# Optimization experiments

Hardware: AMD Instinct MI355X
Metric: run time of the kernel (lower is better)

The kernel has to match this reference:

```python
import jax, jax.numpy as jnp
import numpy as np

N, T, F = 20000, 20, 128
H = 128          # lstm hidden per direction
GH, HEADS = 128, 4
NUM_CLASSES = 10
E = 640000
SCALE = 0.05


def _lstm_last_hidden(x, lengths, Wih, Whh, b):
    """Run a unidirectional LSTM over padded x [N,T,F]; return hidden at the
    last valid step per sequence (torch gate order i,f,g,o)."""
    pre = jnp.einsum('ntf,gf->ntg', x, Wih) + b            # [N,T,4H]
    mask = jnp.arange(x.shape[1])[None, :] < lengths[:, None]  # [N,T]
    h0 = jnp.zeros((x.shape[0], Whh.shape[1]), x.dtype)

    def step(carry, inp):
        h, c = carry
        pt, m = inp                                         # [N,4H], [N]
        gates = pt + h @ Whh.T
        i, f, g, o = jnp.split(gates, 4, axis=-1)
        c_new = jax.nn.sigmoid(f) * c + jax.nn.sigmoid(i) * jnp.tanh(g)
        h_new = jax.nn.sigmoid(o) * jnp.tanh(c_new)
        m = m[:, None]
        return (jnp.where(m, h_new, h), jnp.where(m, c_new, c)), None

    (h, _), _ = jax.lax.scan(step, (h0, h0), (pre.transpose(1, 0, 2), mask.T))
    return h


def _reverse_by_length(x, lengths):
    # x[n, t] -> x[n, len-1-t] for t < len (padding positions are masked later)
    idx = jnp.clip(lengths[:, None] - 1 - jnp.arange(x.shape[1])[None, :], 0, None)
    return x[jnp.arange(x.shape[0])[:, None], idx]


def _gat(h, src, dst, W, a_src, a_dst, bias, heads):
    n = h.shape[0]
    xh = (h @ W.T).reshape(n, heads, -1)                    # [N,H,C]
    al_s = jnp.sum(xh * a_src, -1)                          # [N,H]
    al_d = jnp.sum(xh * a_dst, -1)
    e = jax.nn.leaky_relu(al_s[src] + al_d[dst], 0.2)       # [E,H]
    emax = jax.ops.segment_max(e, dst, num_segments=n)
    emax = jnp.where(jnp.isfinite(emax), emax, 0.0)
    ee = jnp.exp(e - emax[dst])
    denom = jax.ops.segment_sum(ee, dst, num_segments=n)
    alpha = ee / (denom[dst] + 1e-16)                       # segment softmax
    out = jax.ops.segment_sum(xh[src] * alpha[..., None], dst, num_segments=n)
    return out.reshape(n, -1) + bias


def setup_inputs() -> dict:
    key = jax.random.key(0)
    ks = jax.random.split(key, 16)
    p = lambda k, *s: jax.random.normal(k, s, jnp.float32) * SCALE
    return {
        'x': jax.random.normal(ks[0], (N, T, F), jnp.float32),
        'lengths': jax.random.randint(ks[1], (N,), 1, T + 1, jnp.int32),
        'edge_index': jax.random.randint(ks[2], (2, E), 0, N, jnp.int32),
        # BiLSTM params (b = b_ih + b_hh combined; identical math)
        'Wih_f': p(ks[3], 4 * H, F), 'Whh_f': p(ks[4], 4 * H, H), 'b_f': p(ks[5], 4 * H),
        'Wih_b': p(ks[6], 4 * H, F), 'Whh_b': p(ks[7], 4 * H, H), 'b_b': p(ks[8], 4 * H),
        # GAT1: in=2H=256 -> heads*GH=512
        'W1': p(ks[9], HEADS * GH, 2 * H), 'a1_src': p(ks[10], HEADS, GH),
        'a1_dst': p(ks[11], HEADS, GH), 'bias1': jnp.zeros((HEADS * GH,), jnp.float32),
        # GAT2: in=512 -> 1*GH=128
        'W2': p(ks[12], GH, HEADS * GH), 'a2_src': p(ks[13], 1, GH),
        'a2_dst': p(ks[14], 1, GH), 'bias2': jnp.zeros((GH,), jnp.float32),
        'Wfc': p(ks[15], NUM_CLASSES, GH), 'bfc': jnp.zeros((NUM_CLASSES,), jnp.float32),
    }


def reference(x, lengths, edge_index, Wih_f, Whh_f, b_f, Wih_b, Whh_b, b_b,
              W1, a1_src, a1_dst, bias1, W2, a2_src, a2_dst, bias2, Wfc, bfc):
    n = x.shape[0]
    h_fwd = _lstm_last_hidden(x, lengths, Wih_f, Whh_f, b_f)
    h_bwd = _lstm_last_hidden(_reverse_by_length(x, lengths), lengths, Wih_b, Whh_b, b_b)
    h = jnp.concatenate([h_fwd, h_bwd], axis=-1)            # [N, 2H]
    # GATConv default adds self-loops
    loop = jnp.arange(n, dtype=edge_index.dtype)
    src = jnp.concatenate([edge_index[0], loop])
    dst = jnp.concatenate([edge_index[1], loop])
    h = jax.nn.relu(_gat(h, src, dst, W1, a1_src, a1_dst, bias1, HEADS))
    h = jax.nn.relu(_gat(h, src, dst, W2, a2_src, a2_dst, bias2, 1))
    return h @ Wfc.T + bfc                                  # [N, num_classes]
```

## Files before the change

### kernel.cpp

```cpp
#include <hip/hip_runtime.h>

#define NSEQ 20000
#define TT 20
#define FD 128
#define EDG 640000
#define ETOT (EDG + NSEQ)

typedef short bf16x8 __attribute__((ext_vector_type(8)));
typedef float f32x4 __attribute__((ext_vector_type(4)));
typedef unsigned short u16;
typedef unsigned int u32;

__device__ __forceinline__ float bf2f(u16 h) {
  union { u32 u; float f; } v; v.u = ((u32)h) << 16; return v.f;
}
__device__ __forceinline__ float bf_lo(u32 w) {
  union { u32 u; float f; } v; v.u = w << 16; return v.f;
}
__device__ __forceinline__ float bf_hi(u32 w) {
  union { u32 u; float f; } v; v.u = w & 0xffff0000u; return v.f;
}
__device__ __forceinline__ u16 f2bf(float f) {
  union { float f; u32 u; } v; v.f = f;
  u32 u = v.u;
  return (u16)((u + 0x7fffu + ((u >> 16) & 1u)) >> 16);
}
__device__ __forceinline__ float fast_rcp(float x) {
  float r; asm("v_rcp_f32 %0, %1" : "=v"(r) : "v"(x)); return r;
}
__device__ __forceinline__ float fast_ex2(float x) {
  float r; asm("v_exp_f32 %0, %1" : "=v"(r) : "v"(x)); return r;
}
__device__ __forceinline__ u32 cvtpk_bf16(float a, float b) {
  u32 r; asm("v_cvt_pk_bf16_f32 %0, %1, %2" : "=v"(r) : "v"(a), "v"(b)); return r;
}
__device__ __forceinline__ int clampi(int v, int lo, int hi) {
  return v < lo ? lo : (v > hi ? hi : v);
}

template<int BF>
__device__ __forceinline__ bf16x8 ld8(const void* p, size_t i) {
  if (BF) return *(const bf16x8*)((const u16*)p + i);
  f32x4 a = *(const f32x4*)((const float*)p + i);
  f32x4 b = *(const f32x4*)((const float*)p + i + 4);
  union { u32 w[4]; bf16x8 v; } u;
  u.w[0] = cvtpk_bf16(a[0], a[1]);
  u.w[1] = cvtpk_bf16(a[2], a[3]);
  u.w[2] = cvtpk_bf16(b[0], b[1]);
  u.w[3] = cvtpk_bf16(b[2], b[3]);
  return u.v;
}

#define OFF_WIHF 0
#define OFF_WHHF 65536
#define OFF_BF   131072
#define OFF_WIHB 131584
#define OFF_WHHB 197120
#define OFF_BB   262656
#define OFF_W1   263168
#define OFF_W2   394240
#define OFF_A1S  459776
#define OFF_A1D  460288
#define OFF_B1   460800
#define OFF_A2S  461312
#define OFF_A2D  461440
#define OFF_B2   461568
#define OFF_WFC  461696
#define OFF_BFC  462976

__global__ void k_detect_zero(const u32* __restrict__ xw, int* __restrict__ flag,
                              int* __restrict__ deg, int* __restrict__ lcnt) {
  int i = blockIdx.x * 256 + threadIdx.x;
  if (i < NSEQ) deg[i] = 0;
  if (i < 64) lcnt[i] = 0;
  if (blockIdx.x == 0 && threadIdx.x < 64) {
    u16 lo = (u16)(xw[threadIdx.x] & 0xffffu);
    int e = (lo >> 7) & 0xff;
    unsigned long long m = __ballot(e >= 100 && e <= 140);
    if (threadIdx.x == 0) flag[0] = (__popcll(m) >= 32) ? 1 : 0;
  }
}

struct CvtArgs {
  const void* src[16];
  int off[16];
  int cnt[16];
  int wt[16];
};

template<int BF>
__global__ void k_cvt(CvtArgs a, u16* __restrict__ canon, const int* __restrict__ flag) {
  if (flag[0] != BF) return;
  int idx = blockIdx.x * 256 + threadIdx.x;
  int stride = gridDim.x * 256;
#pragma unroll 1
  for (int s = 0; s < 16; ++s) {
    const void* sp = a.src[s];
    int n = a.cnt[s], off = a.off[s], wt = a.wt[s];
    for (int i = idx; i < n; i += stride) {
      float v = BF ? bf2f(((const u16*)sp)[i]) : ((const float*)sp)[i];
      if (wt) {
        int gate = (wt == 1) ? ((i >> 14) & 3) : ((i >> 7) & 3);
        v *= (gate == 2) ? 2.885390082f : -1.442695041f;
      }
      canon[off + i] = f2bf(v);
    }
  }
}

__global__ void k_fill0(u16* __restrict__ out, int n) {
  int i = blockIdx.x * 256 + threadIdx.x;
  if (i < n) out[i] = 0;
}

template<int BF>
__global__ __launch_bounds__(512, 2) void k_lstm(
    const void* __restrict__ x, const int* __restrict__ lengths,
    const int* __restrict__ lperm,
    const u16* __restrict__ canon, u16* __restrict__ hcat,
    const int* __restrict__ flag)
{
  if (flag[0] != BF) return;
  __shared__ u16 Ax[2][64 * 128];
  __shared__ u16 Ah[2][64 * 128];
  __shared__ int lenS[64];
  __shared__ int seqS[64];

  const int tid = threadIdx.x;
  const int wv = tid >> 6;
  const int lane = tid & 63;
  const int q = lane >> 4;
  const int cc = lane & 15;
  const int dir = blockIdx.x;
  const int b0 = (gridDim.y - 1 - blockIdx.y) * 64;

  const u16* Wi = canon + (dir ? OFF_WIHB : OFF_WIHF);
  const u16* Wh = canon + (dir ? OFF_WHHB : OFF_WHHF);
  const u16* bb = canon + (dir ? OFF_BB : OFF_BF);

  bf16x8 wih[4][4], whh[4][4];
  uint2 bvp[4];
#pragma unroll
  for (int g = 0; g < 4; ++g) {
    int row = g * 128 + wv * 16 + cc;
#pragma unroll
    for (int kt = 0; kt < 4; ++kt) {
      wih[g][kt] = *(const bf16x8*)(Wi + row * 128 + kt * 32 + q * 8);
      whh[g][kt] = *(const bf16x8*)(Wh + row * 128 + kt * 32 + q * 8);
    }
    bvp[g] = *(const uint2*)(bb + g * 128 + wv * 16 + q * 4);
  }

  if (tid < 64) {
    int s = lperm[clampi(b0 + tid, 0, NSEQ - 1)];
    s = clampi(s, 0, NSEQ - 1);
    seqS[tid] = s;
    lenS[tid] = clampi(lengths[s], 1, TT);
  }
  {
    f32x4 zz = {0.f, 0.f, 0.f, 0.f};
    f32x4* p = (f32x4*)Ah[0];
    for (int i = tid; i < 1024; i += 512) p[i] = zz;
  }
  __syncthreads();

  const int tmax = lenS[63];

  int lenq[4];
#pragma unroll
  for (int m = 0; m < 4; ++m) lenq[m] = lenS[m * 16 + cc];

  const int lrow = tid >> 3;
  const int lj = tid & 7;
  const int sL = seqS[lrow];
  const int lenL = lenS[lrow];
  const size_t xbase = (size_t)sL * (TT * FD);
  const int ax0 = lrow * 128 + ((lj ^ (lrow & 15)) * 8);
  const int ax1 = lrow * 128 + (((lj + 8) ^ (lrow & 15)) * 8);

  int rofs[4];
#pragma unroll
  for (int kt = 0; kt < 4; ++kt) rofs[kt] = cc * 128 + (((4 * kt + q) ^ cc) * 8);
  const int awbase = cc * 128 + (((wv * 2 + (q >> 1)) ^ cc) * 8) + (q & 1) * 4;

  {
    int t0 = dir ? (lenL - 1) : 0;
    bf16x8 d0 = ld8<BF>(x, xbase + t0 * FD + lj * 8);
    bf16x8 d1 = ld8<BF>(x, xbase + t0 * FD + (lj + 8) * 8);
    *(bf16x8*)&Ax[0][ax0] = d0;
    *(bf16x8*)&Ax[0][ax1] = d1;
  }
  float c[4][4] = {};
  int cb = 0;
  __syncthreads();

#pragma unroll 1
  for (int t = 0; t < tmax; ++t) {
    const u16* Axr = Ax[cb];
    u16* Axw = Ax[cb ^ 1];
    const u16* Ahr = Ah[cb];
    u16* Ahw = Ah[cb ^ 1];

    bf16x8 d0 = {}, d1 = {};
    const bool more = (t + 1 < tmax);
    if (more) {
      int tn = t + 1;
      int tt2 = dir ? (lenL - 1 - tn) : tn;
      if (tt2 < 0) tt2 = 0;
      d0 = ld8<BF>(x, xbase + tt2 * FD + lj * 8);
      d1 = ld8<BF>(x, xbase + tt2 * FD + (lj + 8) * 8);
    }

#pragma unroll
    for (int m = 0; m < 4; ++m) {
      const int mb = m * 2048;
      f32x4 acc[4];
#pragma unroll
      for (int g = 0; g < 4; ++g) {
        f32x4 vi = {bf_lo(bvp[g].x), bf_hi(bvp[g].x), bf_lo(bvp[g].y), bf_hi(bvp[g].y)};
        acc[g] = vi;
      }
#pragma unroll
      for (int kt = 0; kt < 4; ++kt) {
        bf16x8 b = *(const bf16x8*)&Axr[mb + rofs[kt]];
#pragma unroll
        for (int g = 0; g < 4; ++g)
          acc[g] = __builtin_amdgcn_mfma_f32_16x16x32_bf16(wih[g][kt], b, acc[g], 0, 0, 0);
      }
#pragma unroll
      for (int kt = 0; kt < 4; ++kt) {
        bf16x8 b = *(const bf16x8*)&Ahr[mb + rofs[kt]];
#pragma unroll
        for (int g = 0; g < 4; ++g)
          acc[g] = __builtin_amdgcn_mfma_f32_16x16x32_bf16(whh[g][kt], b, acc[g], 0, 0, 0);
      }

      uint2 hw;
      if (t < lenq[m]) {
        float hf[4];
#pragma unroll
        for (int r = 0; r < 4; ++r) {
          float Ei = fast_ex2(acc[0][r]);
          float Ef = fast_ex2(acc[1][r]);
          float G  = fast_ex2(acc[2][r]) + 1.0f;
          float Eo = fast_ex2(acc[3][r]);
          float A = 1.0f + Ef, B = 1.0f + Ei;
          float BG = B * G;
          float num = c[m][r] * BG + (A * G - 2.0f * A);
          float cn = num * fast_rcp(A * BG);
          c[m][r] = cn;
          float C2 = fast_ex2(cn * 2.885390082f) + 1.0f;
          hf[r] = (C2 - 2.0f) * fast_rcp((1.0f + Eo) * C2);
        }
        hw.x = cvtpk_bf16(hf[0], hf[1]);
        hw.y = cvtpk_bf16(hf[2], hf[3]);
      } else {
        hw = *(const uint2*)&Ahr[mb + awbase];
      }
      *(uint2*)&Ahw[mb + awbase] = hw;
    }

    if (more) {
      *(bf16x8*)&Axw[ax0] = d0;
      *(bf16x8*)&Axw[ax1] = d1;
    }
    __syncthreads();
    cb ^= 1;
  }

  for (int i = tid; i < 1024; i += 512) {
    int row = i >> 4, ch = i & 15;
    if (b0 + row < NSEQ) {
      int seq = seqS[row];
      bf16x8 v = *(const bf16x8*)&Ah[cb][row * 128 + ((ch ^ (row & 15)) * 8)];
      *(bf16x8*)(hcat + (size_t)seq * 256 + dir * 128 + ch * 8) = v;
    }
  }
}

__global__ __launch_bounds__(256) void k_gemm(
    const u16* __restrict__ A, const u16* __restrict__ W, u16* __restrict__ C,
    int M, int Nc, int K,
    const u16* __restrict__ aS, const u16* __restrict__ aD,
    float* __restrict__ als, float* __restrict__ ald, int alsStride)
{
  __shared__ u16 As[128 * 64];
  __shared__ u16 Bs[128 * 64];
  const int tid = threadIdx.x;
  const int wv = tid >> 6, lane = tid & 63, q = lane >> 4, cc = lane & 15;
  const int mblk = blockIdx.x * 128, nblk = blockIdx.y * 128;
  const int wm = (wv & 1) * 64, wn = (wv >> 1) * 64;

  f32x4 acc[4][4] = {};

  const int srow = tid >> 1;
  const int sc0 = (tid & 1) * 4;
  int arow_g = mblk + srow; if (arow_g > M - 1) arow_g = M - 1;
  const u16* aptr = A + (size_t)arow_g * K + sc0 * 8;
  const u16* bptr = W + (size_t)(nblk + srow) * K + sc0 * 8;

  for (int k0 = 0; k0 < K; k0 += 64) {
#pragma unroll
    for (int cch = 0; cch < 4; ++cch) {
      bf16x8 av = *(const bf16x8*)(aptr + k0 + cch * 8);
      bf16x8 bvv = *(const bf16x8*)(bptr + k0 + cch * 8);
      int ch = sc0 + cch;
      *(bf16x8*)&As[srow * 64 + ((ch ^ (srow & 7)) * 8)] = av;
      *(bf16x8*)&Bs[srow * 64 + ((ch ^ (srow & 7)) * 8)] = bvv;
    }
    __syncthreads();
#pragma unroll
    for (int kt = 0; kt < 2; ++kt) {
      bf16x8 af[4];
#pragma unroll
      for (int m = 0; m < 4; ++m) {
        int row = wm + m * 16 + cc;
        af[m] = *(const bf16x8*)&As[row * 64 + (((4 * kt + q) ^ (row & 7)) * 8)];
      }
#pragma unroll
      for (int n = 0; n < 4; ++n) {
        int rowb = wn + n * 16 + cc;
        bf16x8 bfr = *(const bf16x8*)&Bs[rowb * 64 + (((4 * kt + q) ^ (rowb & 7)) * 8)];
#pragma unroll
        for (int m = 0; m < 4; ++m)
          acc[m][n] = __builtin_amdgcn_mfma_f32_16x16x32_bf16(bfr, af[m], acc[m][n], 0, 0, 0);
      }
    }
    __syncthreads();
  }

  float pls[4] = {}, pld[4] = {};
#pragma unroll
  for (int n = 0; n < 4; ++n) {
    uint2 ws = *(const uint2*)(aS + nblk + wn + n * 16 + q * 4);
    uint2 wd = *(const uint2*)(aD + nblk + wn + n * 16 + q * 4);
    float s0 = bf_lo(ws.x), s1 = bf_hi(ws.x), s2 = bf_lo(ws.y), s3 = bf_hi(ws.y);
    float d0 = bf_lo(wd.x), d1 = bf_hi(wd.x), d2 = bf_lo(wd.y), d3 = bf_hi(wd.y);
#pragma unroll
    for (int m = 0; m < 4; ++m) {
      int row = mblk + wm + m * 16 + cc;
      uint2 st;
      st.x = cvtpk_bf16(acc[m][n][0], acc[m][n][1]);
      st.y = cvtpk_bf16(acc[m][n][2], acc[m][n][3]);
      if (row < M) *(uint2*)(C + (size_t)row * Nc + nblk + wn + n * 16 + q * 4) = st;
      pls[m] += acc[m][n][0] * s0 + acc[m][n][1] * s1 + acc[m][n][2] * s2 + acc[m][n][3] * s3;
      pld[m] += acc[m][n][0] * d0 + acc[m][n][1] * d1 + acc[m][n][2] * d2 + acc[m][n][3] * d3;
    }
  }

#pragma unroll
  for (int m = 0; m < 4; ++m) {
    pls[m] += __shfl_xor(pls[m], 16, 64);
    pls[m] += __shfl_xor(pls[m], 32, 64);
    pld[m] += __shfl_xor(pld[m], 16, 64);
    pld[m] += __shfl_xor(pld[m], 32, 64);
  }
  float* sred = (float*)As;
  if (lane < 16) {
#pragma unroll
    for (int m = 0; m < 4; ++m) {
      int idx = ((wv & 1) * 4 + m) * 32 + cc * 2 + (wv >> 1);
      sred[idx] = pls[m];
      sred[256 + idx] = pld[m];
    }
  }
  __syncthreads();
  if (wv < 2) {
    int m = lane >> 4, ccc = lane & 15;
    int row = mblk + wv * 64 + m * 16 + ccc;
    int idx = (wv * 4 + m) * 32 + ccc * 2;
    if (row < M) {
      als[(size_t)row * alsStride + blockIdx.y] = sred[idx] + sred[idx + 1];
      ald[(size_t)row * alsStride + blockIdx.y] = sred[256 + idx] + sred[256 + idx + 1];
    }
  }
}

__global__ __launch_bounds__(256) void k_agg1(
    const u16* __restrict__ xh1, const float* __restrict__ als, const float* __restrict__ ald,
    const int* __restrict__ offs, const int* __restrict__ csr,
    const u16* __restrict__ canon, u16* __restrict__ h1)
{
  const int lane = threadIdx.x & 63;
  const int n = blockIdx.x * 4 + (threadIdx.x >> 6);
  int off0 = offs[n], off1 = offs[n + 1];
  off0 = clampi(off0, 0, ETOT);
  off1 = clampi(off1, off0, ETOT);
  const int deg = off1 - off0;
  const float4 ad = *(const float4*)(ald + (size_t)n * 4);
  const u16* xb = xh1 + lane * 2;

  float o0 = 0.f, o1 = 0.f, o2 = 0.f, o3 = 0.f, o4 = 0.f, o5 = 0.f, o6 = 0.f, o7 = 0.f;
  if (deg <= 64) {
    int s = 0;
    float e0 = -1e30f, e1 = -1e30f, e2 = -1e30f, e3 = -1e30f;
    if (lane < deg) {
      s = clampi(csr[off0 + lane], 0, NSEQ - 1);
      float4 av = *(const float4*)(als + (size_t)s * 4);
      float t;
      t = av.x + ad.x; e0 = t > 0.f ? t : 0.2f * t;
      t = av.y + ad.y; e1 = t > 0.f ? t : 0.2f * t;
      t = av.z + ad.z; e2 = t > 0.f ? t : 0.2f * t;
      t = av.w + ad.w; e3 = t > 0.f ? t : 0.2f * t;
    }
    float m0 = e0, m1 = e1, m2 = e2, m3 = e3;
#pragma unroll
    for (int off = 32; off >= 1; off >>= 1) {
      m0 = fmaxf(m0, __shfl_xor(m0, off, 64));
      m1 = fmaxf(m1, __shfl_xor(m1, off, 64));
      m2 = fmaxf(m2, __shfl_xor(m2, off, 64));
      m3 = fmaxf(m3, __shfl_xor(m3, off, 64));
    }
    float x0 = (lane < deg) ? __expf(e0 - m0) : 0.f;
    float x1 = (lane < deg) ? __expf(e1 - m1) : 0.f;
    float x2 = (lane < deg) ? __expf(e2 - m2) : 0.f;
    float x3 = (lane < deg) ? __expf(e3 - m3) : 0.f;
    float s0 = x0, s1 = x1, s2 = x2, s3 = x3;
#pragma unroll
    for (int off = 32; off >= 1; off >>= 1) {
      s0 += __shfl_xor(s0, off, 64);
      s1 += __shfl_xor(s1, off, 64);
      s2 += __shfl_xor(s2, off, 64);
      s3 += __shfl_xor(s3, off, 64);
    }
    float a0 = x0 * fast_rcp(s0 + 1e-16f);
    float a1 = x1 * fast_rcp(s1 + 1e-16f);
    float a2 = x2 * fast_rcp(s2 + 1e-16f);
    float a3 = x3 * fast_rcp(s3 + 1e-16f);
    const int sofs = s * 512;
#pragma unroll 4
    for (int j = 0; j < deg; ++j) {
      int so = __builtin_amdgcn_readlane(sofs, j);
      float aa0 = __int_as_float(__builtin_amdgcn_readlane(__float_as_int(a0), j));
      float aa1 = __int_as_float(__builtin_amdgcn_readlane(__float_as_int(a1), j));
      float aa2 = __int_as_float(__builtin_amdgcn_readlane(__float_as_int(a2), j));
      float aa3 = __int_as_float(__builtin_amdgcn_readlane(__float_as_int(a3), j));
      u32 v0 = *(const u32*)(xb + so);
      u32 v1 = *(const u32*)(xb + so + 128);
      u32 v2 = *(const u32*)(xb + so + 256);
      u32 v3 = *(const u32*)(xb + so + 384);
      o0 += aa0 * bf_lo(v0); o1 += aa0 * bf_hi(v0);
      o2 += aa1 * bf_lo(v1); o3 += aa1 * bf_hi(v1);
      o4 += aa2 * bf_lo(v2); o5 += aa2 * bf_hi(v2);
      o6 += aa3 * bf_lo(v3); o7 += aa3 * bf_hi(v3);
    }
  } else {
    float m0 = -1e30f, m1 = -1e30f, m2 = -1e30f, m3 = -1e30f;
    for (int k = off0 + lane; k < off1; k += 64) {
      int s = clampi(csr[k], 0, NSEQ - 1);
      float4 av = *(const float4*)(als + (size_t)s * 4);
      float t;
      t = av.x + ad.x; t = t > 0.f ? t : 0.2f * t; m0 = fmaxf(m0, t);
      t = av.y + ad.y; t = t > 0.f ? t : 0.2f * t; m1 = fmaxf(m1, t);
      t = av.z + ad.z; t = t > 0.f ? t : 0.2f * t; m2 = fmaxf(m2, t);
      t = av.w + ad.w; t = t > 0.f ? t : 0.2f * t; m3 = fmaxf(m3, t);
    }
#pragma unroll
    for (int off = 32; off >= 1; off >>= 1) {
      m0 = fmaxf(m0, __shfl_xor(m0, off, 64));
      m1 = fmaxf(m1, __shfl_xor(m1, off, 64));
      m2 = fmaxf(m2, __shfl_xor(m2, off, 64));
      m3 = fmaxf(m3, __shfl_xor(m3, off, 64));
    }
    float s0 = 0.f, s1 = 0.f, s2 = 0.f, s3 = 0.f;
    for (int k = off0 + lane; k < off1; k += 64) {
      int s = clampi(csr[k], 0, NSEQ - 1);
      float4 av = *(const float4*)(als + (size_t)s * 4);
      float t;
      t = av.x + ad.x; t = t > 0.f ? t : 0.2f * t; s0 += __expf(t - m0);
      t = av.y + ad.y; t = t > 0.f ? t : 0.2f * t; s1 += __expf(t - m1);
      t = av.z + ad.z; t = t > 0.f ? t : 0.2f * t; s2 += __expf(t - m2);
      t = av.w + ad.w; t = t > 0.f ? t : 0.2f * t; s3 += __expf(t - m3);
    }
#pragma unroll
    for (int off = 32; off >= 1; off >>= 1) {
      s0 += __shfl_xor(s0, off, 64);
      s1 += __shfl_xor(s1, off, 64);
      s2 += __shfl_xor(s2, off, 64);
      s3 += __shfl_xor(s3, off, 64);
    }
    float rd0 = fast_rcp(s0 + 1e-16f), rd1 = fast_rcp(s1 + 1e-16f);
    float rd2 = fast_rcp(s2 + 1e-16f), rd3 = fast_rcp(s3 + 1e-16f);
    for (int k = off0; k < off1; ++k) {
      int s = clampi(csr[k], 0, NSEQ - 1);
      float4 av = *(const float4*)(als + (size_t)s * 4);
      float t;
      t = av.x + ad.x; t = t > 0.f ? t : 0.2f * t; float aa0 = __expf(t - m0) * rd0;
      t = av.y + ad.y; t = t > 0.f ? t : 0.2f * t; float aa1 = __expf(t - m1) * rd1;
      t = av.z + ad.z; t = t > 0.f ? t : 0.2f * t; float aa2 = __expf(t - m2) * rd2;
      t = av.w + ad.w; t = t > 0.f ? t : 0.2f * t; float aa3 = __expf(t - m3) * rd3;
      const u16* xr = xb + (size_t)s * 512;
      u32 v0 = *(const u32*)(xr);
      u32 v1 = *(const u32*)(xr + 128);
      u32 v2 = *(const u32*)(xr + 256);
      u32 v3 = *(const u32*)(xr + 384);
      o0 += aa0 * bf_lo(v0); o1 += aa0 * bf_hi(v0);
      o2 += aa1 * bf_lo(v1); o3 += aa1 * bf_hi(v1);
      o4 += aa2 * bf_lo(v2); o5 += aa2 * bf_hi(v2);
      o6 += aa3 * bf_lo(v3); o7 += aa3 * bf_hi(v3);
    }
  }
  float b0 = bf2f(canon[OFF_B1 + lane * 2]),       b1 = bf2f(canon[OFF_B1 + lane * 2 + 1]);
  float b2 = bf2f(canon[OFF_B1 + 128 + lane * 2]), b3 = bf2f(canon[OFF_B1 + 128 + lane * 2 + 1]);
  float b4 = bf2f(canon[OFF_B1 + 256 + lane * 2]), b5 = bf2f(canon[OFF_B1 + 256 + lane * 2 + 1]);
  float b6 = bf2f(canon[OFF_B1 + 384 + lane * 2]), b7 = bf2f(canon[OFF_B1 + 384 + lane * 2 + 1]);
  o0 += b0; o1 += b1; o2 += b2; o3 += b3; o4 += b4; o5 += b5; o6 += b6; o7 += b7;
  o0 = o0 > 0.f ? o0 : 0.f; o1 = o1 > 0.f ? o1 : 0.f;
  o2 = o2 > 0.f ? o2 : 0.f; o3 = o3 > 0.f ? o3 : 0.f;
  o4 = o4 > 0.f ? o4 : 0.f; o5 = o5 > 0.f ? o5 : 0.f;
  o6 = o6 > 0.f ? o6 : 0.f; o7 = o7 > 0.f ? o7 : 0.f;
  u16* hb = h1 + (size_t)n * 512 + lane * 2;
  *(u32*)(hb)       = cvtpk_bf16(o0, o1);
  *(u32*)(hb + 128) = cvtpk_bf16(o2, o3);
  *(u32*)(hb + 256) = cvtpk_bf16(o4, o5);
  *(u32*)(hb + 384) = cvtpk_bf16(o6, o7);
}

__global__ __launch_bounds__(256) void k_agg2(
    const u16* __restrict__ xh2, const float* __restrict__ als2, const float* __restrict__ ald2,
    const int* __restrict__ offs, const int* __restrict__ csr,
    const u16* __restrict__ canon, void* __restrict__ out, const int* __restrict__ flag)
{
  const int lane = threadIdx.x & 63;
  const int n = blockIdx.x * 4 + (threadIdx.x >> 6);
  int off0 = offs[n], off1 = offs[n + 1];
  off0 = clampi(off0, 0, ETOT);
  off1 = clampi(off1, off0, ETOT);
  const float adn = ald2[n];
  const int deg = off1 - off0;

  float o0 = 0.f, o1 = 0.f;
  if (deg <= 64) {
    int s = 0;
    float e = -1e30f;
    if (lane < deg) {
      s = clampi(csr[off0 + lane], 0, NSEQ - 1);
      float t = als2[s] + adn;
      e = t > 0.f ? t : 0.2f * t;
    }
    float mx = e;
#pragma unroll
    for (int off = 32; off >= 1; off >>= 1) mx = fmaxf(mx, __shfl_xor(mx, off, 64));
    float ex = (lane < deg) ? __expf(e - mx) : 0.f;
    float sm = ex;
#pragma unroll
    for (int off = 32; off >= 1; off >>= 1) sm += __shfl_xor(sm, off, 64);
    const float a = ex * fast_rcp(sm + 1e-16f);
    const int sofs = s * 128;
#pragma unroll 4
    for (int j = 0; j < deg; ++j) {
      int so = __builtin_amdgcn_readlane(sofs, j);
      float aa = __int_as_float(__builtin_amdgcn_readlane(__float_as_int(a), j));
      u32 xv = *(const u32*)(xh2 + so + lane * 2);
      o0 += aa * bf_lo(xv);
      o1 += aa * bf_hi(xv);
    }
  } else {
    float mx = -1e30f;
    for (int k = off0 + lane; k < off1; k += 64) {
      float e = als2[clampi(csr[k], 0, NSEQ - 1)] + adn;
      e = e > 0.f ? e : 0.2f * e;
      mx = fmaxf(mx, e);
    }
#pragma unroll
    for (int off = 32; off >= 1; off >>= 1) mx = fmaxf(mx, __shfl_xor(mx, off, 64));
    float sm = 0.f;
    for (int k = off0 + lane; k < off1; k += 64) {
      float e = als2[clampi(csr[k], 0, NSEQ - 1)] + adn;
      e = e > 0.f ? e : 0.2f * e;
      sm += __expf(e - mx);
    }
#pragma unroll
    for (int off = 32; off >= 1; off >>= 1) sm += __shfl_xor(sm, off, 64);
    float rd = fast_rcp(sm + 1e-16f);
#pragma unroll 4
    for (int k = off0; k < off1; ++k) {
      int s = clampi(csr[k], 0, NSEQ - 1);
      float e = als2[s] + adn;
      e = e > 0.f ? e : 0.2f * e;
      float a = __expf(e - mx) * rd;
      u32 xv = *(const u32*)(xh2 + (size_t)s * 128 + lane * 2);
      o0 += a * bf_lo(xv);
      o1 += a * bf_hi(xv);
    }
  }
  o0 += bf2f(canon[OFF_B2 + lane * 2]);     o0 = o0 > 0.f ? o0 : 0.f;
  o1 += bf2f(canon[OFF_B2 + lane * 2 + 1]); o1 = o1 > 0.f ? o1 : 0.f;

  float res[10];
#pragma unroll
  for (int cls = 0; cls < 10; ++cls) {
    float p = o0 * bf2f(canon[OFF_WFC + cls * 128 + lane * 2]) +
              o1 * bf2f(canon[OFF_WFC + cls * 128 + lane * 2 + 1]);
#pragma unroll
    for (int off = 32; off >= 1; off >>= 1) p += __shfl_xor(p, off, 64);
    float v = p + bf2f(canon[OFF_BFC + cls]);
    res[cls] = (fabsf(v) < 1e30f) ? v : 0.f;
  }
  if (flag[0]) {
    if (lane < 5) {
      u32 pk = (u32)f2bf(res[lane * 2]) | ((u32)f2bf(res[lane * 2 + 1]) << 16);
      ((u32*)out)[(size_t)n * 5 + lane] = pk;
    }
  } else {
    if (lane < 10) ((float*)out)[(size_t)n * 10 + lane] = res[lane];
  }
}

__global__ void k_hist_all(const int* __restrict__ ei, const int* __restrict__ lengths,
                           int* __restrict__ deg, int* __restrict__ lcnt) {
  int i = blockIdx.x * 256 + threadIdx.x;
  if (i < ETOT) {
    int d = (i < EDG) ? ei[EDG + i] : (i - EDG);
    d = clampi(d, 0, NSEQ - 1);
    atomicAdd(&deg[d], 1);
  }
  if (i < NSEQ) atomicAdd(&lcnt[clampi(lengths[i], 1, TT) - 1], 1);
}

__global__ __launch_bounds__(1024) void k_scan(const int* __restrict__ deg,
                                               int* __restrict__ offs, int* __restrict__ cur,
                                               const int* __restrict__ lcnt,
                                               int* __restrict__ lcur) {
  __shared__ int wsum[16];
  const int tid = threadIdx.x;
  if (tid == 0) {
    int run = 0;
    for (int i = 0; i < TT; ++i) { lcur[i] = run; run += lcnt[i]; }
  }
  const int lane = tid & 63, wv = tid >> 6;
  const int CHUNK = 20;
  int base = tid * CHUNK;
  int loc[20];
  int s = 0;
#pragma unroll
  for (int i = 0; i < CHUNK; ++i) {
    int idx = base + i;
    int v = (idx < NSEQ) ? deg[idx] : 0;
    loc[i] = s;
    s += v;
  }
  int inc = s;
#pragma unroll
  for (int off = 1; off < 64; off <<= 1) {
    int t2 = __shfl_up(inc, off, 64);
    if (lane >= off) inc += t2;
  }
  if (lane == 63) wsum[wv] = inc;
  __syncthreads();
  int wbase = 0;
  for (int i = 0; i < wv; ++i) wbase += wsum[i];
  int tbase = wbase + inc - s;
#pragma unroll
  for (int i = 0; i < CHUNK; ++i) {
    int idx = base + i;
    if (idx < NSEQ) {
      int st = tbase + loc[i];
      offs[idx] = st;
      cur[idx] = st;
    }
  }
  if (tid == 0) offs[NSEQ] = ETOT;
}

__global__ void k_scatter_all(const int* __restrict__ ei, const int* __restrict__ lengths,
                              int* __restrict__ cur, int* __restrict__ csr,
                              int* __restrict__ lcur, int* __restrict__ lperm) {
  int i = blockIdx.x * 256 + threadIdx.x;
  if (i < ETOT) {
    int s, d;
    if (i < EDG) { s = ei[i]; d = ei[EDG + i]; }
    else { s = i - EDG; d = s; }
    d = clampi(d, 0, NSEQ - 1);
    int pos = atomicAdd(&cur[d], 1);
    pos = clampi(pos, 0, ETOT - 1);
    csr[pos] = s;
  }
  if (i < NSEQ) {
    int b = clampi(lengths[i], 1, TT) - 1;
    int pos = atomicAdd(&lcur[b], 1);
    lperm[clampi(pos, 0, NSEQ - 1)] = i;
  }
}

extern "C" void kernel_launch(void* const* d_in, const int* in_sizes, int n_in,
                              void* d_out, int out_size, void* d_ws, size_t ws_size,
                              hipStream_t stream) {
  (void)in_sizes; (void)n_in;
  const void* x     = d_in[0];
  const int* lengths= (const int*)d_in[1];
  const int* ei     = (const int*)d_in[2];

  const size_t NEED = 45769344u;
  if (ws_size < NEED) {
    k_fill0<<<(out_size + 255) / 256, 256, 0, stream>>>((u16*)d_out, out_size);
    return;
  }

  char* w = (char*)d_ws;
  size_t o = 0;
  auto alloc = [&](size_t b) { char* p = w + o; o += (b + 255) & ~(size_t)255; return p; };
  int*  flag = (int*)  alloc(256);
  u16*  canon= (u16*)  alloc(1048576);
  int*  deg  = (int*)  alloc((size_t)NSEQ * 4);
  int*  offs = (int*)  alloc((size_t)(NSEQ + 1) * 4);
  int*  cur  = (int*)  alloc((size_t)NSEQ * 4);
  int*  csr  = (int*)  alloc((size_t)ETOT * 4);
  float* als1= (float*)alloc((size_t)NSEQ * 4 * 4);
  float* ald1= (float*)alloc((size_t)NSEQ * 4 * 4);
  char* regB = alloc((size_t)NSEQ * 512 * 2);
  u16*  xh1  = (u16*)regB;
  u16*  xh2  = (u16*)regB;
  float* als2= (float*)(regB + (size_t)NSEQ * 128 * 2 + (size_t)NSEQ * 128 * 4);
  float* ald2= als2 + NSEQ;
  char* regA = alloc((size_t)NSEQ * 256 * 2);
  u16*  hcat = (u16*)regA;
  u16*  h1   = (u16*)regA;
  alloc((size_t)NSEQ * 256 * 2);

  int* lperm = (int*)regB;
  int* lcnt  = (int*)(regB + 80128);
  int* lcur  = (int*)(regB + 80256);

  k_detect_zero<<<(NSEQ + 255) / 256, 256, 0, stream>>>((const u32*)x, flag, deg, lcnt);

  CvtArgs ca;
  const int srcIdx[16] = {3, 4, 5, 6, 7, 8, 9, 13, 10, 11, 12, 14, 15, 16, 17, 18};
  const int offv[16]   = {OFF_WIHF, OFF_WHHF, OFF_BF, OFF_WIHB, OFF_WHHB, OFF_BB,
                          OFF_W1, OFF_W2, OFF_A1S, OFF_A1D, OFF_B1,
                          OFF_A2S, OFF_A2D, OFF_B2, OFF_WFC, OFF_BFC};
  const int cntv[16]   = {65536, 65536, 512, 65536, 65536, 512,
                          131072, 65536, 512, 512, 512, 128, 128, 128, 1280, 10};
  const int wtv[16]    = {1, 1, 2, 1, 1, 2, 0, 0, 0, 0, 0, 0, 0, 0, 0, 0};
  for (int i = 0; i < 16; ++i) {
    ca.src[i] = d_in[srcIdx[i]]; ca.off[i] = offv[i]; ca.cnt[i] = cntv[i]; ca.wt[i] = wtv[i];
  }
  k_cvt<1><<<256, 256, 0, stream>>>(ca, canon, flag);
  k_cvt<0><<<256, 256, 0, stream>>>(ca, canon, flag);

  k_hist_all<<<(ETOT + 255) / 256, 256, 0, stream>>>(ei, lengths, deg, lcnt);
  k_scan<<<1, 1024, 0, stream>>>(deg, offs, cur, lcnt, lcur);
  k_scatter_all<<<(ETOT + 255) / 256, 256, 0, stream>>>(ei, lengths, cur, csr, lcur, lperm);

  k_lstm<1><<<dim3(2, 313), 512, 0, stream>>>(x, lengths, lperm, canon, hcat, flag);
  k_lstm<0><<<dim3(2, 313), 512, 0, stream>>>(x, lengths, lperm, canon, hcat, flag);

  k_gemm<<<dim3(157, 4), 256, 0, stream>>>(hcat, canon + OFF_W1, xh1, NSEQ, 512, 256,
                                           canon + OFF_A1S, canon + OFF_A1D, als1, ald1, 4);
  k_agg1<<<5000, 256, 0, stream>>>(xh1, als1, ald1, offs, csr, canon, h1);

  k_gemm<<<dim3(157, 1), 256, 0, stream>>>(h1, canon + OFF_W2, xh2, NSEQ, 128, 512,
                                           canon + OFF_A2S, canon + OFF_A2D, als2, ald2, 1);
  k_agg2<<<5000, 256, 0, stream>>>(xh2, als2, ald2, offs, csr, canon, d_out, flag);
}
```

Baseline: 748.1 us.

## Interleave GAT1 feature layout so aggregation uses 16-byte gathers

The first GEMM now stores xh1 in a permuted column order that places each lane's eight head values contiguously. GAT1 aggregation can then fetch one 16-byte vector per neighbor instead of four scattered 4-byte loads, and h1 is stored the same way. To keep the second GEMM correct, the W2 columns and bias1 are permuted to match during weight conversion. The GEMM epilogue's stores become strided 4-byte writes, which may cost some write efficiency.

```diff
diff --git a/kernel.cpp b/kernel.cpp
--- a/kernel.cpp
+++ b/kernel.cpp
@@ -10,6 +10,7 @@
 typedef float f32x4 __attribute__((ext_vector_type(4)));
 typedef unsigned short u16;
 typedef unsigned int u32;
+typedef unsigned int u32x4 __attribute__((ext_vector_type(4)));
 
 __device__ __forceinline__ float bf2f(u16 h) {
   union { u32 u; float f; } v; v.u = ((u32)h) << 16; return v.f;
@@ -68,6 +69,10 @@
 #define OFF_WFC  461696
 #define OFF_BFC  462976
 
+__device__ __forceinline__ int perm512(int k) {
+  return ((k & 126) << 2) + ((k >> 7) << 1) + (k & 1);
+}
+
 __global__ void k_detect_zero(const u32* __restrict__ xw, int* __restrict__ flag,
                               int* __restrict__ deg, int* __restrict__ lcnt) {
   int i = blockIdx.x * 256 + threadIdx.x;
@@ -99,11 +104,14 @@
     int n = a.cnt[s], off = a.off[s], wt = a.wt[s];
     for (int i = idx; i < n; i += stride) {
       float v = BF ? bf2f(((const u16*)sp)[i]) : ((const float*)sp)[i];
-      if (wt) {
+      if (wt == 1 || wt == 2) {
         int gate = (wt == 1) ? ((i >> 14) & 3) : ((i >> 7) & 3);
         v *= (gate == 2) ? 2.885390082f : -1.442695041f;
       }
-      canon[off + i] = f2bf(v);
+      int di = i;
+      if (wt == 3) di = (i & ~511) | perm512(i & 511);
+      else if (wt == 4) di = perm512(i);
+      canon[off + di] = f2bf(v);
     }
   }
 }
@@ -282,7 +290,7 @@
     const u16* __restrict__ A, const u16* __restrict__ W, u16* __restrict__ C,
     int M, int Nc, int K,
     const u16* __restrict__ aS, const u16* __restrict__ aD,
-    float* __restrict__ als, float* __restrict__ ald, int alsStride)
+    float* __restrict__ als, float* __restrict__ ald, int alsStride, int permStore)
 {
   __shared__ u16 As[128 * 64];
   __shared__ u16 Bs[128 * 64];
@@ -342,7 +350,16 @@
       uint2 st;
       st.x = cvtpk_bf16(acc[m][n][0], acc[m][n][1]);
       st.y = cvtpk_bf16(acc[m][n][2], acc[m][n][3]);
-      if (row < M) *(uint2*)(C + (size_t)row * Nc + nblk + wn + n * 16 + q * 4) = st;
+      if (row < M) {
+        if (permStore) {
+          int f = wn + n * 16 + q * 4;
+          u32* dst = (u32*)(C + (size_t)row * Nc + ((f >> 1) << 3) + (nblk >> 6));
+          dst[0] = st.x;
+          dst[4] = st.y;
+        } else {
+          *(uint2*)(C + (size_t)row * Nc + nblk + wn + n * 16 + q * 4) = st;
+        }
+      }
       pls[m] += acc[m][n][0] * s0 + acc[m][n][1] * s1 + acc[m][n][2] * s2 + acc[m][n][3] * s3;
       pld[m] += acc[m][n][0] * d0 + acc[m][n][1] * d1 + acc[m][n][2] * d2 + acc[m][n][3] * d3;
     }
@@ -388,7 +405,7 @@
   off1 = clampi(off1, off0, ETOT);
   const int deg = off1 - off0;
   const float4 ad = *(const float4*)(ald + (size_t)n * 4);
-  const u16* xb = xh1 + lane * 2;
+  const u16* xb = xh1 + lane * 8;
 
   float o0 = 0.f, o1 = 0.f, o2 = 0.f, o3 = 0.f, o4 = 0.f, o5 = 0.f, o6 = 0.f, o7 = 0.f;
   if (deg <= 64) {
@@ -435,14 +452,11 @@
       float aa1 = __int_as_float(__builtin_amdgcn_readlane(__float_as_int(a1), j));
       float aa2 = __int_as_float(__builtin_amdgcn_readlane(__float_as_int(a2), j));
       float aa3 = __int_as_float(__builtin_amdgcn_readlane(__float_as_int(a3), j));
-      u32 v0 = *(const u32*)(xb + so);
-      u32 v1 = *(const u32*)(xb + so + 128);
-      u32 v2 = *(const u32*)(xb + so + 256);
-      u32 v3 = *(const u32*)(xb + so + 384);
-      o0 += aa0 * bf_lo(v0); o1 += aa0 * bf_hi(v0);
-      o2 += aa1 * bf_lo(v1); o3 += aa1 * bf_hi(v1);
-      o4 += aa2 * bf_lo(v2); o5 += aa2 * bf_hi(v2);
-      o6 += aa3 * bf_lo(v3); o7 += aa3 * bf_hi(v3);
+      u32x4 v = *(const u32x4*)(xb + so);
+      o0 += aa0 * bf_lo(v.x); o1 += aa0 * bf_hi(v.x);
+      o2 += aa1 * bf_lo(v.y); o3 += aa1 * bf_hi(v.y);
+      o4 += aa2 * bf_lo(v.z); o5 += aa2 * bf_hi(v.z);
+      o6 += aa3 * bf_lo(v.w); o7 += aa3 * bf_hi(v.w);
     }
   } else {
     float m0 = -1e30f, m1 = -1e30f, m2 = -1e30f, m3 = -1e30f;
@@ -489,31 +503,28 @@
       t = av.y + ad.y; t = t > 0.f ? t : 0.2f * t; float aa1 = __expf(t - m1) * rd1;
       t = av.z + ad.z; t = t > 0.f ? t : 0.2f * t; float aa2 = __expf(t - m2) * rd2;
       t = av.w + ad.w; t = t > 0.f ? t : 0.2f * t; float aa3 = __expf(t - m3) * rd3;
-      const u16* xr = xb + (size_t)s * 512;
-      u32 v0 = *(const u32*)(xr);
-      u32 v1 = *(const u32*)(xr + 128);
-      u32 v2 = *(const u32*)(xr + 256);
-      u32 v3 = *(const u32*)(xr + 384);
-      o0 += aa0 * bf_lo(v0); o1 += aa0 * bf_hi(v0);
-      o2 += aa1 * bf_lo(v1); o3 += aa1 * bf_hi(v1);
-      o4 += aa2 * bf_lo(v2); o5 += aa2 * bf_hi(v2);
-      o6 += aa3 * bf_lo(v3); o7 += aa3 * bf_hi(v3);
-    }
-  }
-  float b0 = bf2f(canon[OFF_B1 + lane * 2]),       b1 = bf2f(canon[OFF_B1 + lane * 2 + 1]);
-  float b2 = bf2f(canon[OFF_B1 + 128 + lane * 2]), b3 = bf2f(canon[OFF_B1 + 128 + lane * 2 + 1]);
-  float b4 = bf2f(canon[OFF_B1 + 256 + lane * 2]), b5 = bf2f(canon[OFF_B1 + 256 + lane * 2 + 1]);
-  float b6 = bf2f(canon[OFF_B1 + 384 + lane * 2]), b7 = bf2f(canon[OFF_B1 + 384 + lane * 2 + 1]);
-  o0 += b0; o1 += b1; o2 += b2; o3 += b3; o4 += b4; o5 += b5; o6 += b6; o7 += b7;
+      u32x4 v = *(const u32x4*)(xb + (size_t)s * 512);
+      o0 += aa0 * bf_lo(v.x); o1 += aa0 * bf_hi(v.x);
+      o2 += aa1 * bf_lo(v.y); o3 += aa1 * bf_hi(v.y);
+      o4 += aa2 * bf_lo(v.z); o5 += aa2 * bf_hi(v.z);
+      o6 += aa3 * bf_lo(v.w); o7 += aa3 * bf_hi(v.w);
+    }
+  }
+  u32x4 bv = *(const u32x4*)(canon + OFF_B1 + lane * 8);
+  o0 += bf_lo(bv.x); o1 += bf_hi(bv.x);
+  o2 += bf_lo(bv.y); o3 += bf_hi(bv.y);
+  o4 += bf_lo(bv.z); o5 += bf_hi(bv.z);
+  o6 += bf_lo(bv.w); o7 += bf_hi(bv.w);
   o0 = o0 > 0.f ? o0 : 0.f; o1 = o1 > 0.f ? o1 : 0.f;
   o2 = o2 > 0.f ? o2 : 0.f; o3 = o3 > 0.f ? o3 : 0.f;
   o4 = o4 > 0.f ? o4 : 0.f; o5 = o5 > 0.f ? o5 : 0.f;
   o6 = o6 > 0.f ? o6 : 0.f; o7 = o7 > 0.f ? o7 : 0.f;
-  u16* hb = h1 + (size_t)n * 512 + lane * 2;
-  *(u32*)(hb)       = cvtpk_bf16(o0, o1);
-  *(u32*)(hb + 128) = cvtpk_bf16(o2, o3);
-  *(u32*)(hb + 256) = cvtpk_bf16(o4, o5);
-  *(u32*)(hb + 384) = cvtpk_bf16(o6, o7);
+  u32x4 st;
+  st.x = cvtpk_bf16(o0, o1);
+  st.y = cvtpk_bf16(o2, o3);
+  st.z = cvtpk_bf16(o4, o5);
+  st.w = cvtpk_bf16(o6, o7);
+  *(u32x4*)(h1 + (size_t)n * 512 + lane * 8) = st;
 }
 
 __global__ __launch_bounds__(256) void k_agg2(
@@ -731,7 +742,7 @@
                           OFF_A2S, OFF_A2D, OFF_B2, OFF_WFC, OFF_BFC};
   const int cntv[16]   = {65536, 65536, 512, 65536, 65536, 512,
                           131072, 65536, 512, 512, 512, 128, 128, 128, 1280, 10};
-  const int wtv[16]    = {1, 1, 2, 1, 1, 2, 0, 0, 0, 0, 0, 0, 0, 0, 0, 0};
+  const int wtv[16]    = {1, 1, 2, 1, 1, 2, 0, 3, 0, 0, 4, 0, 0, 0, 0, 0};
   for (int i = 0; i < 16; ++i) {
     ca.src[i] = d_in[srcIdx[i]]; ca.off[i] = offv[i]; ca.cnt[i] = cntv[i]; ca.wt[i] = wtv[i];
   }
@@ -746,10 +757,10 @@
   k_lstm<0><<<dim3(2, 313), 512, 0, stream>>>(x, lengths, lperm, canon, hcat, flag);
 
   k_gemm<<<dim3(157, 4), 256, 0, stream>>>(hcat, canon + OFF_W1, xh1, NSEQ, 512, 256,
-                                           canon + OFF_A1S, canon + OFF_A1D, als1, ald1, 4);
+                                           canon + OFF_A1S, canon + OFF_A1D, als1, ald1, 4, 1);
   k_agg1<<<5000, 256, 0, stream>>>(xh1, als1, ald1, offs, csr, canon, h1);
 
   k_gemm<<<dim3(157, 1), 256, 0, stream>>>(h1, canon + OFF_W2, xh2, NSEQ, 128, 512,
-                                           canon + OFF_A2S, canon + OFF_A2D, als2, ald2, 1);
+                                           canon + OFF_A2S, canon + OFF_A2D, als2, ald2, 1, 0);
   k_agg2<<<5000, 256, 0, stream>>>(xh2, als2, ald2, offs, csr, canon, d_out, flag);
 }
```

After: 765.4 us. +2.3%, slower.
